# Performance work log

Hardware: AMD Instinct MI355X
Metric: run time of the kernel (lower is better)

Reference implementation:

```python
import jax, jax.numpy as jnp
import numpy as np

N_V, N_H, T, B = 1024, 512, 128, 256


def setup_inputs() -> dict:
    key = jax.random.key(0)
    k = jax.random.split(key, 3)
    v_data = (jax.random.uniform(k[0], (N_V, T, B)) < 0.5).astype(jnp.float32)  # binary visibles
    W = 0.01 * jax.random.normal(k[1], (N_H, N_V), jnp.float32)
    U = 0.01 * jax.random.normal(k[2], (N_H, N_H), jnp.float32)
    b_h = jnp.zeros((N_H,), jnp.float32)
    b_init = jnp.zeros((N_H,), jnp.float32)
    b_v = jnp.zeros((N_V,), jnp.float32)
    return {"v_data": v_data, "W": W, "U": U, "b_h": b_h, "b_init": b_init,
            "b_v": b_v, "CDk": 2}


def _sample_r_over_time(v, W, U, b_h, b_init):
    # v: (V,T,B) -> r: (H,T,B). Sequential mean-field recurrence over T
    # (RTRBM._sample_r_given_v_over_time: t=0 uses b_init and U=0, t>0 uses U,b_h).
    Wv = jnp.einsum('hv,vtb->thb', W, v)  # (T,H,B)
    r0 = jax.nn.sigmoid(Wv[0] + b_init[:, None])

    def step(r_lag, wv_t):
        r_t = jax.nn.sigmoid(wv_t + U @ r_lag + b_h[:, None])
        return r_t, r_t

    _, rs = jax.lax.scan(step, r0, Wv[1:])
    r = jnp.concatenate([r0[None], rs], axis=0)  # (T,H,B)
    return jnp.transpose(r, (1, 0, 2))  # (H,T,B)


def _parallel_r(v, r_lagged, W, U, b_h, b_init):
    # RTRBM._parallel_sample_r_h_given_v probabilities; v:(V,T,B), r_lagged:(H,T,B)
    r0 = jax.nn.sigmoid(jnp.einsum('hv,vb->hb', W, v[:, 0]) + b_init[:, None])
    rr = jax.nn.sigmoid(jnp.einsum('hv,vtb->htb', W, v[:, 1:])
                        + jnp.einsum('hr,rtb->htb', U, r_lagged[:, :-1])
                        + b_h[:, None, None])
    return jnp.concatenate([r0[:, None], rr], axis=1)  # (H,T,B)


def reference(v_data, W, U, b_h, b_init, b_v, CDk):
    key = jax.random.key(42)
    r_data = _sample_r_over_time(v_data, W, U, b_h, b_init)
    key, sk = jax.random.split(key)
    h_model = jax.random.bernoulli(sk, _parallel_r(v_data, r_data, W, U, b_h, b_init)).astype(v_data.dtype)
    for _ in range(CDk - 1):  # CD-k Gibbs chain (CDk is a concrete Python int)
        key, k1, k2 = jax.random.split(key, 3)
        v_prob = jax.nn.sigmoid(jnp.einsum('hv,htb->vtb', W, h_model) + b_v[:, None, None])
        v_model = jax.random.bernoulli(k1, v_prob).astype(v_data.dtype)
        h_model = jax.random.bernoulli(k2, _parallel_r(v_model, r_data, W, U, b_h, b_init)).astype(v_data.dtype)
    key, kf = jax.random.split(key)
    v_model = jax.random.bernoulli(
        kf, jax.nn.sigmoid(jnp.einsum('hv,htb->vtb', W, h_model) + b_v[:, None, None])
    ).astype(v_data.dtype)
    return (v_model, r_data)
```

## Files before the change

### kernel.cpp

```cpp
#include <hip/hip_runtime.h>
#include <hip/hip_bf16.h>
#include <stdint.h>

typedef unsigned long long u64;
typedef uint32_t u32;
typedef __attribute__((ext_vector_type(8))) short bf16x8;
typedef __attribute__((ext_vector_type(4))) float f32x4;

#define NV 1024
#define NH 512
#define TT 128
#define BB 256
#define TBsz (TT*BB)
#define HTBsz (NH*TBsz)
#define VTBsz (NV*TBsz)
#define NWV (NV/64)
#define NWH (NH/64)
#define QCAP 1048576u
#define DELTA 5e-4

__host__ __device__ inline void tf2x32(uint32_t k0, uint32_t k1,
                                       uint32_t x0, uint32_t x1,
                                       uint32_t& o0, uint32_t& o1) {
  const uint32_t ks2 = k0 ^ k1 ^ 0x1BD11BDAu;
#define ROTL(x,d) (((x)<<(d))|((x)>>(32-(d))))
#define RND(r) { x0 += x1; x1 = ROTL(x1,r); x1 ^= x0; }
  x0 += k0;  x1 += k1;
  RND(13) RND(15) RND(26) RND(6)
  x0 += k1;  x1 += ks2 + 1u;
  RND(17) RND(29) RND(16) RND(24)
  x0 += ks2; x1 += k0 + 2u;
  RND(13) RND(15) RND(26) RND(6)
  x0 += k0;  x1 += k1 + 3u;
  RND(17) RND(29) RND(16) RND(24)
  x0 += k1;  x1 += ks2 + 4u;
  RND(13) RND(15) RND(26) RND(6)
  x0 += ks2; x1 += k0 + 5u;
  o0 = x0; o1 = x1;
#undef RND
#undef ROTL
}

__device__ inline double tf_uniform64(uint32_t k0, uint32_t k1, uint32_t i) {
  uint32_t o0, o1;
  tf2x32(k0, k1, 0u, i, o0, o1);
  uint32_t bits = o0 ^ o1;
  uint32_t fb = (bits >> 9) | 0x3f800000u;
  float f = __uint_as_float(fb) - 1.0f;
  return (double)f;
}

__device__ inline double sigmoid64(double x) { return 1.0 / (1.0 + exp(-x)); }

__device__ inline void bfsplit(float w, ushort& b1o, ushort& b2o) {
  __hip_bfloat16 b1 = __float2bfloat16(w);
  float r = w - __bfloat162float(b1);
  __hip_bfloat16 b2 = __float2bfloat16(r);
  b1o = *reinterpret_cast<ushort*>(&b1);
  b2o = *reinterpret_cast<ushort*>(&b2);
}

__global__ __launch_bounds__(256) void kprepWall(const float* __restrict__ W,
                                                 double* __restrict__ W64,
                                                 ushort* __restrict__ A1,
                                                 ushort* __restrict__ A2,
                                                 ushort* __restrict__ AW1,
                                                 ushort* __restrict__ AW2) {
  int idx = blockIdx.x * 256 + threadIdx.x;
  W64[idx] = (double)W[idx];
  {
    int i    = idx & 7;
    int lane = (idx >> 3) & 63;
    int ks   = (idx >> 9) & 15;
    int vt   = idx >> 13;
    int h = ks*32 + ((lane >> 4) << 3) + i;
    int v = vt*16 + (lane & 15);
    bfsplit(W[(size_t)h*NV + v], A1[idx], A2[idx]);
  }
  {
    int i    = idx & 7;
    int lane = (idx >> 3) & 63;
    int kt   = (idx >> 9) & 31;
    int ht   = idx >> 14;
    int h = ht*16 + (lane & 15);
    int v = kt*32 + ((lane >> 4) << 3) + i;
    bfsplit(W[(size_t)h*NV + v], AW1[idx], AW2[idx]);
  }
}

__global__ __launch_bounds__(256) void kprepUall(const float* __restrict__ U,
                                                 double* __restrict__ U64,
                                                 float4* __restrict__ UB,
                                                 ushort* __restrict__ AU1,
                                                 ushort* __restrict__ AU2) {
  int idx = blockIdx.x * 256 + threadIdx.x;
  U64[idx] = (double)U[idx];
  {
    int i    = idx & 7;
    int lane = (idx >> 3) & 63;
    int kt   = (idx >> 9) & 15;
    int ht   = idx >> 13;
    int h = ht*16 + (lane & 15);
    int r = kt*32 + ((lane >> 4) << 3) + i;
    bfsplit(U[(size_t)h*NH + r], AU1[idx], AU2[idx]);
  }
  if (idx < NH*NH/4) {
    int r4 = idx / NH;
    int h  = idx % NH;
    const float* __restrict__ p = U + (size_t)h*NH + r4*4;
    UB[idx] = make_float4(p[0], p[1], p[2], p[3]);
  }
}

__global__ __launch_bounds__(256) void kpack_f32(const float* __restrict__ in,
                                                 u64* __restrict__ out) {
  int tb = blockIdx.x * 256 + threadIdx.x;
  for (int w = 0; w < NWV; ++w) {
    u64 m = 0;
    #pragma unroll 8
    for (int j = 0; j < 64; ++j)
      m |= (u64)(in[(size_t)(w*64 + j)*TBsz + tb] != 0.0f ? 1 : 0) << j;
    out[(size_t)tb*NWV + w] = m;
  }
}

__global__ __launch_bounds__(256) void kWv(const u64* __restrict__ vb,
                                           const double* __restrict__ W64,
                                           double* __restrict__ WvT) {
  const int HM = 8;
  int t  = blockIdx.x / (NH/HM);
  int h0 = (blockIdx.x % (NH/HM)) * HM;
  int tb = t*BB + threadIdx.x;
  u64 m[NWV];
  #pragma unroll
  for (int w = 0; w < NWV; ++w) m[w] = vb[(size_t)tb*NWV + w];
  double acc[HM];
  #pragma unroll
  for (int i = 0; i < HM; ++i) acc[i] = 0.0;
  const double2* __restrict__ W2 = (const double2*)W64;
  for (int w = 0; w < NWV; ++w) {
    u64 mw = m[w];
    #pragma unroll 8
    for (int j2 = 0; j2 < 32; ++j2) {
      double bd0 = (double)((unsigned)((mw >> (2*j2+0)) & 1ull));
      double bd1 = (double)((unsigned)((mw >> (2*j2+1)) & 1ull));
      int vi = w*32 + j2;
      #pragma unroll
      for (int i = 0; i < HM; ++i) {
        double2 wv = W2[(size_t)(h0+i)*(NV/2) + vi];
        acc[i] = fma(bd0, wv.x, acc[i]);
        acc[i] = fma(bd1, wv.y, acc[i]);
      }
    }
  }
  #pragma unroll
  for (int i = 0; i < HM; ++i)
    WvT[(size_t)tb*NH + h0 + i] = acc[i];
}

__global__ __launch_bounds__(512) void krecur(const double* __restrict__ WvT,
                                              const float4* __restrict__ UB,
                                              const float* __restrict__ bh,
                                              const float* __restrict__ binit,
                                              double* __restrict__ rT) {
  __shared__ double rA[2][NH];
  const int b = blockIdx.x;
  const int h = threadIdx.x;
  const double bhd = (double)bh[h];
  double p = sigmoid64(WvT[(size_t)b*NH + h] + (double)binit[h]);
  rA[0][h] = p;
  rT[(size_t)b*NH + h] = p;
  __syncthreads();
  int cur = 0;
  for (int t = 1; t < TT; ++t) {
    double acc = WvT[((size_t)t*BB + b)*NH + h];
    double a0=0, a1=0, a2=0, a3=0;
    const double2* __restrict__ xl = (const double2*)rA[cur];
    const double2* __restrict__ xg =
        (const double2*)(rT + ((size_t)(t-1)*BB + b)*NH);
    #pragma unroll 4
    for (int r = 0; r < 256; r += 4) {
      float4 u4 = UB[(size_t)(r >> 2)*NH + h];
      double2 q01 = xl[(r>>1)+0];
      double2 q23 = xl[(r>>1)+1];
      a0 = fma((double)u4.x, q01.x, a0);
      a1 = fma((double)u4.y, q01.y, a1);
      a2 = fma((double)u4.z, q23.x, a2);
      a3 = fma((double)u4.w, q23.y, a3);
    }
    #pragma unroll 4
    for (int r = 256; r < 512; r += 4) {
      float4 u4 = UB[(size_t)(r >> 2)*NH + h];
      double2 q01 = xg[(r>>1)+0];
      double2 q23 = xg[(r>>1)+1];
      a0 = fma((double)u4.x, q01.x, a0);
      a1 = fma((double)u4.y, q01.y, a1);
      a2 = fma((double)u4.z, q23.x, a2);
      a3 = fma((double)u4.w, q23.y, a3);
    }
    p = sigmoid64((acc + ((a0+a1)+(a2+a3))) + bhd);
    rA[cur ^ 1][h] = p;
    rT[((size_t)t*BB + b)*NH + h] = p;
    __syncthreads();
    cur ^= 1;
  }
}

__global__ __launch_bounds__(256) void ktrans_s(const double* __restrict__ rT,
                                                float* __restrict__ out_r,
                                                uint8_t* __restrict__ hbytes,
                                                u32 k0, u32 k1) {
  __shared__ double lds[32][33];
  int t  = blockIdx.x;
  int h0 = blockIdx.y * 32;
  int b0 = blockIdx.z * 32;
  int tx = threadIdx.x & 31;
  int ty = threadIdx.x >> 5;
  #pragma unroll
  for (int i = 0; i < 4; ++i) {
    int row = ty*4 + i;
    lds[row][tx] = rT[((size_t)t*BB + b0 + row)*NH + h0 + tx];
  }
  __syncthreads();
  #pragma unroll
  for (int i = 0; i < 4; ++i) {
    int row = ty*4 + i;
    out_r[(size_t)(h0+row)*TBsz + (size_t)t*BB + b0 + tx] = (float)lds[tx][row];
  }
  if (threadIdx.x < 128) {
    int tbr = threadIdx.x >> 2;
    int bix = threadIdx.x & 3;
    int tb  = t*BB + b0 + tbr;
    unsigned byte = 0;
    #pragma unroll
    for (int j = 0; j < 8; ++j) {
      int hrel = bix*8 + j;
      double p = lds[tbr][hrel];
      double u = tf_uniform64(k0, k1, (u32)((h0 + hrel)*TBsz + tb));
      byte |= (u < p) ? (1u << j) : 0u;
    }
    hbytes[(size_t)tb*(NH/8) + (h0 >> 3) + bix] = (uint8_t)byte;
  }
}

__global__ __launch_bounds__(256) void kvisM(
    const ushort* __restrict__ A1, const ushort* __restrict__ A2,
    const float* __restrict__ bv, const u64* __restrict__ hbits,
    u64* __restrict__ vbits, float* __restrict__ vf,
    u32* __restrict__ queue, u32* __restrict__ cnt, u32 k0, u32 k1) {
  __shared__ ushort Blds[64*512];
  int nblk = blockIdx.x & 511;
  int vblk = blockIdx.x >> 9;
  int tb0 = nblk * 64, v0 = vblk * 64;
  int tid = threadIdx.x;
  {
    int c = tid >> 2, seg = tid & 3;
    const u64* hp = hbits + (size_t)(tb0 + c)*NWH + seg*2;
    #pragma unroll
    for (int half = 0; half < 2; ++half) {
      u64 mm = hp[half];
      int kbase = seg*128 + half*64;
      #pragma unroll
      for (int j2 = 0; j2 < 32; ++j2) {
        int k = kbase + 2*j2;
        u32 val = (u32)((mm >> (2*j2)) & 1ull) * 0x3F80u
                | (u32)((mm >> (2*j2+1)) & 1ull) * 0x3F800000u;
        int blk = (k >> 3) ^ (c & 7);
        *(u32*)&Blds[c*512 + (blk << 3) + (k & 7)] = val;
      }
    }
  }
  __syncthreads();
  int wv = tid >> 6, l = tid & 63;
  int wr = wv >> 1, wc = wv & 1;
  f32x4 acc[2][2];
  #pragma unroll
  for (int m = 0; m < 2; ++m)
    #pragma unroll
    for (int n = 0; n < 2; ++n) acc[m][n] = (f32x4){0.f,0.f,0.f,0.f};
  for (int ks = 0; ks < 16; ++ks) {
    bf16x8 bf[2];
    #pragma unroll
    for (int n = 0; n < 2; ++n) {
      int col = wc*32 + n*16 + (l & 15);
      int k = ks*32 + ((l >> 4) << 3);
      int blk = (k >> 3) ^ (col & 7);
      bf[n] = *(const bf16x8*)&Blds[col*512 + (blk << 3)];
    }
    #pragma unroll
    for (int m = 0; m < 2; ++m) {
      int vt = vblk*4 + wr*2 + m;
      size_t abase = (((size_t)vt*16 + ks)*64 + l)*8;
      bf16x8 a1 = *(const bf16x8*)&A1[abase];
      bf16x8 a2 = *(const bf16x8*)&A2[abase];
      #pragma unroll
      for (int n = 0; n < 2; ++n) {
        acc[m][n] = __builtin_amdgcn_mfma_f32_16x16x32_bf16(a1, bf[n], acc[m][n], 0,0,0);
        acc[m][n] = __builtin_amdgcn_mfma_f32_16x16x32_bf16(a2, bf[n], acc[m][n], 0,0,0);
      }
    }
  }
  u64 mask[2] = {0, 0};
  int coln[2];
  #pragma unroll
  for (int n = 0; n < 2; ++n) {
    int col = wc*32 + n*16 + (l & 15);
    coln[n] = col;
    int tb = tb0 + col;
    #pragma unroll
    for (int m = 0; m < 2; ++m) {
      #pragma unroll
      for (int r = 0; r < 4; ++r) {
        int vrel = wr*32 + m*16 + ((l >> 4) << 2) + r;
        int v = v0 + vrel;
        float p = 1.f / (1.f + __expf(-(acc[m][n][r] + bv[v])));
        size_t o = (size_t)v*TBsz + tb;
        double u = tf_uniform64(k0, k1, (u32)o);
        double diff = (double)p - u;
        unsigned smp = diff > 0.0 ? 1u : 0u;
        if (fabs(diff) < DELTA) {
          u32 s = atomicAdd(cnt, 1u);
          if (s < QCAP) queue[s] = (u32)o;
        }
        if (smp) mask[n] |= 1ull << vrel;
        if (vf) vf[o] = (float)smp;
      }
    }
  }
  if (vbits) {
    __syncthreads();
    u64* sbits = (u64*)Blds;
    if (tid < 64) sbits[tid] = 0;
    __syncthreads();
    atomicOr(&sbits[coln[0]], mask[0]);
    atomicOr(&sbits[coln[1]], mask[1]);
    __syncthreads();
    if (tid < 64)
      vbits[(size_t)(tb0 + tid)*NWV + (v0 >> 6)] = sbits[tid];
  }
}

__global__ __launch_bounds__(256) void khidM(
    const ushort* __restrict__ AW1, const ushort* __restrict__ AW2,
    const ushort* __restrict__ AU1, const ushort* __restrict__ AU2,
    const float* __restrict__ bh, const float* __restrict__ binit,
    const u64* __restrict__ vbits, const float* __restrict__ r32,
    u64* __restrict__ h2bits, u32* __restrict__ queue,
    u32* __restrict__ cnt, u32 k0, u32 k1) {
  __shared__ ushort Blds[64*512];
  int nblk = blockIdx.x & 511;
  int hblk = blockIdx.x >> 9;
  int tb0 = nblk * 64, h0 = hblk * 64;
  int t = tb0 >> 8;
  int tid = threadIdx.x;
  int wv = tid >> 6, l = tid & 63;
  int wr = wv >> 1, wc = wv & 1;
  f32x4 acc[2][2];
  #pragma unroll
  for (int m = 0; m < 2; ++m)
    #pragma unroll
    for (int n = 0; n < 2; ++n) acc[m][n] = (f32x4){0.f,0.f,0.f,0.f};

  for (int q = 0; q < 2; ++q) {
    {
      int c = tid >> 2, seg = tid & 3;
      const u64* vp = vbits + (size_t)(tb0 + c)*NWV + q*8 + seg*2;
      #pragma unroll
      for (int half = 0; half < 2; ++half) {
        u64 mm = vp[half];
        int kbase = seg*128 + half*64;
        #pragma unroll
        for (int j2 = 0; j2 < 32; ++j2) {
          int k = kbase + 2*j2;
          u32 val = (u32)((mm >> (2*j2)) & 1ull) * 0x3F80u
                  | (u32)((mm >> (2*j2+1)) & 1ull) * 0x3F800000u;
          int blk = (k >> 3) ^ (c & 7);
          *(u32*)&Blds[c*512 + (blk << 3) + (k & 7)] = val;
        }
      }
    }
    __syncthreads();
    for (int ks = 0; ks < 16; ++ks) {
      int kt = q*16 + ks;
      bf16x8 bf[2];
      #pragma unroll
      for (int n = 0; n < 2; ++n) {
        int col = wc*32 + n*16 + (l & 15);
        int k = ks*32 + ((l >> 4) << 3);
        int blk = (k >> 3) ^ (col & 7);
        bf[n] = *(const bf16x8*)&Blds[col*512 + (blk << 3)];
      }
      #pragma unroll
      for (int m = 0; m < 2; ++m) {
        int ht = hblk*4 + wr*2 + m;
        size_t abase = (((size_t)ht*32 + kt)*64 + l)*8;
        bf16x8 a1 = *(const bf16x8*)&AW1[abase];
        bf16x8 a2 = *(const bf16x8*)&AW2[abase];
        #pragma unroll
        for (int n = 0; n < 2; ++n) {
          acc[m][n] = __builtin_amdgcn_mfma_f32_16x16x32_bf16(a1, bf[n], acc[m][n], 0,0,0);
          acc[m][n] = __builtin_amdgcn_mfma_f32_16x16x32_bf16(a2, bf[n], acc[m][n], 0,0,0);
        }
      }
    }
    __syncthreads();
  }

  if (t > 0) {
    int tbl0 = tb0 - 256;
    for (int pl = 0; pl < 2; ++pl) {
      {
        int c  = tid & 63;
        int q4 = tid >> 6;
        const float* __restrict__ rp = r32 + tbl0 + c;
        for (int rr = 0; rr < 128; ++rr) {
          int r = q4*128 + rr;
          float x = rp[(size_t)r*TBsz];
          __hip_bfloat16 b1 = __float2bfloat16(x);
          ushort ub;
          if (pl == 0) {
            ub = *reinterpret_cast<ushort*>(&b1);
          } else {
            float res = x - __bfloat162float(b1);
            __hip_bfloat16 b2 = __float2bfloat16(res);
            ub = *reinterpret_cast<ushort*>(&b2);
          }
          int blk = (r >> 3) ^ (c & 7);
          Blds[c*512 + (blk << 3) + (r & 7)] = ub;
        }
      }
      __syncthreads();
      for (int ks = 0; ks < 16; ++ks) {
        bf16x8 bf[2];
        #pragma unroll
        for (int n = 0; n < 2; ++n) {
          int col = wc*32 + n*16 + (l & 15);
          int k = ks*32 + ((l >> 4) << 3);
          int blk = (k >> 3) ^ (col & 7);
          bf[n] = *(const bf16x8*)&Blds[col*512 + (blk << 3)];
        }
        #pragma unroll
        for (int m = 0; m < 2; ++m) {
          int ht = hblk*4 + wr*2 + m;
          size_t abase = (((size_t)ht*16 + ks)*64 + l)*8;
          bf16x8 a1 = *(const bf16x8*)&AU1[abase];
          bf16x8 a2 = *(const bf16x8*)&AU2[abase];
          #pragma unroll
          for (int n = 0; n < 2; ++n) {
            acc[m][n] = __builtin_amdgcn_mfma_f32_16x16x32_bf16(a1, bf[n], acc[m][n], 0,0,0);
            acc[m][n] = __builtin_amdgcn_mfma_f32_16x16x32_bf16(a2, bf[n], acc[m][n], 0,0,0);
          }
        }
      }
      __syncthreads();
    }
  }

  const float* __restrict__ bias = (t > 0) ? bh : binit;
  u64 mask[2] = {0, 0};
  int coln[2];
  #pragma unroll
  for (int n = 0; n < 2; ++n) {
    int col = wc*32 + n*16 + (l & 15);
    coln[n] = col;
    int tb = tb0 + col;
    #pragma unroll
    for (int m = 0; m < 2; ++m) {
      #pragma unroll
      for (int r = 0; r < 4; ++r) {
        int hrel = wr*32 + m*16 + ((l >> 4) << 2) + r;
        int h = h0 + hrel;
        float p = 1.f / (1.f + __expf(-(acc[m][n][r] + bias[h])));
        size_t o = (size_t)h*TBsz + tb;
        double u = tf_uniform64(k0, k1, (u32)o);
        double diff = (double)p - u;
        unsigned smp = diff > 0.0 ? 1u : 0u;
        if (fabs(diff) < DELTA) {
          u32 s = atomicAdd(cnt, 1u);
          if (s < QCAP) queue[s] = (u32)o;
        }
        if (smp) mask[n] |= 1ull << hrel;
      }
    }
  }
  __syncthreads();
  u64* sbits = (u64*)Blds;
  if (tid < 64) sbits[tid] = 0;
  __syncthreads();
  atomicOr(&sbits[coln[0]], mask[0]);
  atomicOr(&sbits[coln[1]], mask[1]);
  __syncthreads();
  if (tid < 64)
    h2bits[(size_t)(tb0 + tid)*NWH + hblk] = sbits[tid];
}

__global__ __launch_bounds__(256) void kvis_fix(
    const float* __restrict__ W, const float* __restrict__ bv,
    const u64* __restrict__ hbits, u64* __restrict__ fixbits,
    float* __restrict__ vf, const u32* __restrict__ queue,
    const u32* __restrict__ cnt, u32 k0, u32 k1) {
  u32 n = *cnt; if (n > QCAP) n = QCAP;
  for (u32 q = blockIdx.x*256 + threadIdx.x; q < n; q += gridDim.x*256) {
    u32 o = queue[q];
    u32 v = o / TBsz, tb = o % TBsz;
    double a0=0, a1=0, a2=0, a3=0;
    for (int w = 0; w < NWH; ++w) {
      u64 mw = hbits[(size_t)tb*NWH + w];
      for (int j = 0; j < 64; j += 4) {
        if ((mw >> (j+0)) & 1ull) a0 += (double)W[(size_t)(w*64+j+0)*NV + v];
        if ((mw >> (j+1)) & 1ull) a1 += (double)W[(size_t)(w*64+j+1)*NV + v];
        if ((mw >> (j+2)) & 1ull) a2 += (double)W[(size_t)(w*64+j+2)*NV + v];
        if ((mw >> (j+3)) & 1ull) a3 += (double)W[(size_t)(w*64+j+3)*NV + v];
      }
    }
    double p = sigmoid64(((a0+a1)+(a2+a3)) + (double)bv[v]);
    double u = tf_uniform64(k0, k1, o);
    unsigned smp = (u < p) ? 1u : 0u;
    if (vf) vf[o] = (float)smp;
    if (fixbits) {
      size_t wi = (size_t)tb*NWV + (v >> 6);
      unsigned bit = v & 63u;
      unsigned cur = (unsigned)((fixbits[wi] >> bit) & 1ull);
      if (cur != smp) atomicXor(&fixbits[wi], 1ull << bit);
    }
  }
}

__global__ __launch_bounds__(256) void khid_fix(
    const u64* __restrict__ vbits, const float* __restrict__ W,
    const double* __restrict__ U64, const float* __restrict__ bh,
    const float* __restrict__ binit, const double* __restrict__ rT,
    u64* __restrict__ fixbits, const u32* __restrict__ queue,
    const u32* __restrict__ cnt, u32 k0, u32 k1) {
  u32 n = *cnt; if (n > QCAP) n = QCAP;
  for (u32 q = blockIdx.x*256 + threadIdx.x; q < n; q += gridDim.x*256) {
    u32 o = queue[q];
    u32 h = o / TBsz, tb = o % TBsz;
    u32 t = tb / BB, b = tb % BB;
    double a0=0, a1=0, a2=0, a3=0;
    for (int w = 0; w < NWV; ++w) {
      u64 mw = vbits[(size_t)tb*NWV + w];
      for (int j = 0; j < 64; j += 4) {
        if ((mw >> (j+0)) & 1ull) a0 += (double)W[(size_t)h*NV + w*64+j+0];
        if ((mw >> (j+1)) & 1ull) a1 += (double)W[(size_t)h*NV + w*64+j+1];
        if ((mw >> (j+2)) & 1ull) a2 += (double)W[(size_t)h*NV + w*64+j+2];
        if ((mw >> (j+3)) & 1ull) a3 += (double)W[(size_t)h*NV + w*64+j+3];
      }
    }
    double logit = (a0+a1) + (a2+a3);
    if (t > 0) {
      const double* __restrict__ rp = rT + ((size_t)(t-1)*BB + b)*NH;
      const double* __restrict__ Ur = U64 + (size_t)h*NH;
      double u0=0, u1=0, u2=0, u3=0;
      for (int r = 0; r < NH; r += 4) {
        u0 = fma(Ur[r+0], rp[r+0], u0);
        u1 = fma(Ur[r+1], rp[r+1], u1);
        u2 = fma(Ur[r+2], rp[r+2], u2);
        u3 = fma(Ur[r+3], rp[r+3], u3);
      }
      logit = (logit + ((u0+u1)+(u2+u3))) + (double)bh[h];
    } else {
      logit += (double)binit[h];
    }
    double p = sigmoid64(logit);
    double u = tf_uniform64(k0, k1, o);
    unsigned smp = (u < p) ? 1u : 0u;
    size_t wi = (size_t)tb*NWH + (h >> 6);
    unsigned bit = h & 63u;
    unsigned cur = (unsigned)((fixbits[wi] >> bit) & 1ull);
    if (cur != smp) atomicXor(&fixbits[wi], 1ull << bit);
  }
}

extern "C" void kernel_launch(void* const* d_in, const int* in_sizes, int n_in,
                              void* d_out, int out_size, void* d_ws, size_t ws_size,
                              hipStream_t stream) {
  const float* vd    = (const float*)d_in[0];
  const float* W     = (const float*)d_in[1];
  const float* U     = (const float*)d_in[2];
  const float* bh    = (const float*)d_in[3];
  const float* binit = (const float*)d_in[4];
  const float* bv    = (const float*)d_in[5];

  float* out_v = (float*)d_out;
  float* out_r = (float*)d_out + VTBsz;
  double* WvT = (double*)d_out;

  char* w = (char*)d_ws;
  double* rT    = (double*)w;  w += (size_t)HTBsz*8;
  u64* vdbits   = (u64*)w;     w += (size_t)TBsz*NWV*8;
  u64* v1bits   = (u64*)w;     w += (size_t)TBsz*NWV*8;
  u64* h1bits   = (u64*)w;     w += (size_t)TBsz*NWH*8;
  u64* h2bits   = (u64*)w;     w += (size_t)TBsz*NWH*8;
  double* W64   = (double*)w;  w += (size_t)NH*NV*8;
  double* U64   = (double*)w;  w += (size_t)NH*NH*8;
  float4* UB    = (float4*)w;  w += (size_t)NH*NH*4;
  ushort* A1    = (ushort*)w;  w += (size_t)NH*NV*2;
  ushort* A2    = (ushort*)w;  w += (size_t)NH*NV*2;
  ushort* AW1   = (ushort*)w;  w += (size_t)NH*NV*2;
  ushort* AW2   = (ushort*)w;  w += (size_t)NH*NV*2;
  ushort* AU1   = (ushort*)w;  w += (size_t)NH*NH*2;
  ushort* AU2   = (ushort*)w;  w += (size_t)NH*NH*2;
  u32* q0       = (u32*)w;     w += (size_t)QCAP*4;
  u32* q1       = (u32*)w;     w += (size_t)QCAP*4;
  u32* q2       = (u32*)w;     w += (size_t)QCAP*4;
  u32* cnt      = (u32*)w;     w += 256;
  (void)ws_size; (void)in_sizes; (void)n_in; (void)out_size;

  uint32_t ka0,ka1, sk0,sk1;
  tf2x32(0u,42u, 0u,0u, ka0,ka1);
  tf2x32(0u,42u, 0u,1u, sk0,sk1);
  uint32_t kb0,kb1, k10,k11, k20,k21;
  tf2x32(ka0,ka1, 0u,0u, kb0,kb1);
  tf2x32(ka0,ka1, 0u,1u, k10,k11);
  tf2x32(ka0,ka1, 0u,2u, k20,k21);
  uint32_t kc0,kc1, kf0,kf1;
  tf2x32(kb0,kb1, 0u,0u, kc0,kc1);
  tf2x32(kb0,kb1, 0u,1u, kf0,kf1);

  hipMemsetAsync(cnt, 0, 3*sizeof(u32), stream);

  kprepWall<<<(NH*NV)/256, 256, 0, stream>>>(W, W64, A1, A2, AW1, AW2);
  kprepUall<<<(NH*NH)/256, 256, 0, stream>>>(U, U64, UB, AU1, AU2);
  kpack_f32<<<TBsz/256, 256, 0, stream>>>(vd, vdbits);

  kWv<<<TT*(NH/8), 256, 0, stream>>>(vdbits, W64, WvT);

  krecur<<<BB, NH, 0, stream>>>(WvT, UB, bh, binit, rT);

  ktrans_s<<<dim3(TT, NH/32, BB/32), 256, 0, stream>>>(rT, out_r,
                                                       (uint8_t*)h1bits, sk0, sk1);

  kvisM<<<16*512, 256, 0, stream>>>(A1, A2, bv, h1bits, v1bits, nullptr,
                                    q0, cnt+0, k10, k11);
  kvis_fix<<<128, 256, 0, stream>>>(W, bv, h1bits, v1bits, nullptr,
                                    q0, cnt+0, k10, k11);

  khidM<<<8*512, 256, 0, stream>>>(AW1, AW2, AU1, AU2, bh, binit,
                                   v1bits, out_r, h2bits, q1, cnt+1, k20, k21);
  khid_fix<<<128, 256, 0, stream>>>(v1bits, W, U64, bh, binit, rT,
                                    h2bits, q1, cnt+1, k20, k21);

  kvisM<<<16*512, 256, 0, stream>>>(A1, A2, bv, h2bits, nullptr, out_v,
                                    q2, cnt+2, kf0, kf1);
  kvis_fix<<<128, 256, 0, stream>>>(W, bv, h2bits, nullptr, out_v,
                                    q2, cnt+2, kf0, kf1);
}
```

Measured before the change: 5.745 ms.

## Make kvisM loop over all visible blocks per column tile and use LDS in recurrence

kvisM now gives each block 128 tb columns and loops over all 16 visible blocks, so the unpacked hidden-bit tile in LDS is built once and reused across the whole visible dimension. The old version rebuilt a 64-column tile for every (v-block, column-block) pair. The launch shrinks to 256 blocks, each holding about 128KB of LDS, so each CU likely runs a single block of 4 waves with little latency hiding. Separately, the recurrence kernel now reads the whole previous r vector from LDS instead of taking half of it from global memory.

```diff
diff --git a/kernel.cpp b/kernel.cpp
--- a/kernel.cpp
+++ b/kernel.cpp
@@ -175,24 +175,12 @@
   for (int t = 1; t < TT; ++t) {
     double acc = WvT[((size_t)t*BB + b)*NH + h];
     double a0=0, a1=0, a2=0, a3=0;
-    const double2* __restrict__ xl = (const double2*)rA[cur];
-    const double2* __restrict__ xg =
-        (const double2*)(rT + ((size_t)(t-1)*BB + b)*NH);
+    const double2* __restrict__ rA2 = (const double2*)rA[cur];
     #pragma unroll 4
-    for (int r = 0; r < 256; r += 4) {
+    for (int r = 0; r < NH; r += 4) {
       float4 u4 = UB[(size_t)(r >> 2)*NH + h];
-      double2 q01 = xl[(r>>1)+0];
-      double2 q23 = xl[(r>>1)+1];
-      a0 = fma((double)u4.x, q01.x, a0);
-      a1 = fma((double)u4.y, q01.y, a1);
-      a2 = fma((double)u4.z, q23.x, a2);
-      a3 = fma((double)u4.w, q23.y, a3);
-    }
-    #pragma unroll 4
-    for (int r = 256; r < 512; r += 4) {
-      float4 u4 = UB[(size_t)(r >> 2)*NH + h];
-      double2 q01 = xg[(r>>1)+0];
-      double2 q23 = xg[(r>>1)+1];
+      double2 q01 = rA2[(r>>1)+0];
+      double2 q23 = rA2[(r>>1)+1];
       a0 = fma((double)u4.x, q01.x, a0);
       a1 = fma((double)u4.y, q01.y, a1);
       a2 = fma((double)u4.z, q23.x, a2);
@@ -248,18 +236,18 @@
     const float* __restrict__ bv, const u64* __restrict__ hbits,
     u64* __restrict__ vbits, float* __restrict__ vf,
     u32* __restrict__ queue, u32* __restrict__ cnt, u32 k0, u32 k1) {
-  __shared__ ushort Blds[64*512];
-  int nblk = blockIdx.x & 511;
-  int vblk = blockIdx.x >> 9;
-  int tb0 = nblk * 64, v0 = vblk * 64;
+  __shared__ ushort Blds[128*512];
+  __shared__ u64 sbits[128];
+  int tb0 = blockIdx.x * 128;
   int tid = threadIdx.x;
   {
-    int c = tid >> 2, seg = tid & 3;
-    const u64* hp = hbits + (size_t)(tb0 + c)*NWH + seg*2;
+    int c  = tid & 127;
+    int hs = tid >> 7;
+    const u64* hp = hbits + (size_t)(tb0 + c)*NWH + hs*4;
     #pragma unroll
-    for (int half = 0; half < 2; ++half) {
-      u64 mm = hp[half];
-      int kbase = seg*128 + half*64;
+    for (int w = 0; w < 4; ++w) {
+      u64 mm = hp[w];
+      int kbase = hs*256 + w*64;
       #pragma unroll
       for (int j2 = 0; j2 < 32; ++j2) {
         int k = kbase + 2*j2;
@@ -273,70 +261,73 @@
   __syncthreads();
   int wv = tid >> 6, l = tid & 63;
   int wr = wv >> 1, wc = wv & 1;
-  f32x4 acc[2][2];
-  #pragma unroll
-  for (int m = 0; m < 2; ++m)
+  for (int vblk = 0; vblk < 16; ++vblk) {
+    f32x4 acc[2][4];
     #pragma unroll
-    for (int n = 0; n < 2; ++n) acc[m][n] = (f32x4){0.f,0.f,0.f,0.f};
-  for (int ks = 0; ks < 16; ++ks) {
-    bf16x8 bf[2];
+    for (int m = 0; m < 2; ++m)
+      #pragma unroll
+      for (int n = 0; n < 4; ++n) acc[m][n] = (f32x4){0.f,0.f,0.f,0.f};
+    for (int ks = 0; ks < 16; ++ks) {
+      bf16x8 bf[4];
+      #pragma unroll
+      for (int n = 0; n < 4; ++n) {
+        int col = wc*64 + n*16 + (l & 15);
+        int k = ks*32 + ((l >> 4) << 3);
+        int blk = (k >> 3) ^ (col & 7);
+        bf[n] = *(const bf16x8*)&Blds[col*512 + (blk << 3)];
+      }
+      #pragma unroll
+      for (int m = 0; m < 2; ++m) {
+        int vt = vblk*4 + wr*2 + m;
+        size_t abase = (((size_t)vt*16 + ks)*64 + l)*8;
+        bf16x8 a1 = *(const bf16x8*)&A1[abase];
+        bf16x8 a2 = *(const bf16x8*)&A2[abase];
+        #pragma unroll
+        for (int n = 0; n < 4; ++n) {
+          acc[m][n] = __builtin_amdgcn_mfma_f32_16x16x32_bf16(a1, bf[n], acc[m][n], 0,0,0);
+          acc[m][n] = __builtin_amdgcn_mfma_f32_16x16x32_bf16(a2, bf[n], acc[m][n], 0,0,0);
+        }
+      }
+    }
+    int v0 = vblk * 64;
+    u64 mask[4] = {0,0,0,0};
     #pragma unroll
-    for (int n = 0; n < 2; ++n) {
-      int col = wc*32 + n*16 + (l & 15);
-      int k = ks*32 + ((l >> 4) << 3);
-      int blk = (k >> 3) ^ (col & 7);
-      bf[n] = *(const bf16x8*)&Blds[col*512 + (blk << 3)];
-    }
-    #pragma unroll
-    for (int m = 0; m < 2; ++m) {
-      int vt = vblk*4 + wr*2 + m;
-      size_t abase = (((size_t)vt*16 + ks)*64 + l)*8;
-      bf16x8 a1 = *(const bf16x8*)&A1[abase];
-      bf16x8 a2 = *(const bf16x8*)&A2[abase];
-      #pragma unroll
-      for (int n = 0; n < 2; ++n) {
-        acc[m][n] = __builtin_amdgcn_mfma_f32_16x16x32_bf16(a1, bf[n], acc[m][n], 0,0,0);
-        acc[m][n] = __builtin_amdgcn_mfma_f32_16x16x32_bf16(a2, bf[n], acc[m][n], 0,0,0);
-      }
-    }
-  }
-  u64 mask[2] = {0, 0};
-  int coln[2];
-  #pragma unroll
-  for (int n = 0; n < 2; ++n) {
-    int col = wc*32 + n*16 + (l & 15);
-    coln[n] = col;
-    int tb = tb0 + col;
-    #pragma unroll
-    for (int m = 0; m < 2; ++m) {
-      #pragma unroll
-      for (int r = 0; r < 4; ++r) {
-        int vrel = wr*32 + m*16 + ((l >> 4) << 2) + r;
-        int v = v0 + vrel;
-        float p = 1.f / (1.f + __expf(-(acc[m][n][r] + bv[v])));
-        size_t o = (size_t)v*TBsz + tb;
-        double u = tf_uniform64(k0, k1, (u32)o);
-        double diff = (double)p - u;
-        unsigned smp = diff > 0.0 ? 1u : 0u;
-        if (fabs(diff) < DELTA) {
-          u32 s = atomicAdd(cnt, 1u);
-          if (s < QCAP) queue[s] = (u32)o;
-        }
-        if (smp) mask[n] |= 1ull << vrel;
-        if (vf) vf[o] = (float)smp;
-      }
-    }
-  }
-  if (vbits) {
-    __syncthreads();
-    u64* sbits = (u64*)Blds;
-    if (tid < 64) sbits[tid] = 0;
-    __syncthreads();
-    atomicOr(&sbits[coln[0]], mask[0]);
-    atomicOr(&sbits[coln[1]], mask[1]);
-    __syncthreads();
-    if (tid < 64)
-      vbits[(size_t)(tb0 + tid)*NWV + (v0 >> 6)] = sbits[tid];
+    for (int n = 0; n < 4; ++n) {
+      int col = wc*64 + n*16 + (l & 15);
+      int tb = tb0 + col;
+      #pragma unroll
+      for (int m = 0; m < 2; ++m) {
+        #pragma unroll
+        for (int r = 0; r < 4; ++r) {
+          int vrel = wr*32 + m*16 + ((l >> 4) << 2) + r;
+          int v = v0 + vrel;
+          float p = 1.f / (1.f + __expf(-(acc[m][n][r] + bv[v])));
+          size_t o = (size_t)v*TBsz + tb;
+          double u = tf_uniform64(k0, k1, (u32)o);
+          double diff = (double)p - u;
+          unsigned smp = diff > 0.0 ? 1u : 0u;
+          if (fabs(diff) < DELTA) {
+            u32 s = atomicAdd(cnt, 1u);
+            if (s < QCAP) queue[s] = (u32)o;
+          }
+          if (smp) mask[n] |= 1ull << vrel;
+          if (vf) vf[o] = (float)smp;
+        }
+      }
+    }
+    if (vbits) {
+      __syncthreads();
+      if (tid < 128) sbits[tid] = 0;
+      __syncthreads();
+      #pragma unroll
+      for (int n = 0; n < 4; ++n) {
+        int col = wc*64 + n*16 + (l & 15);
+        atomicOr(&sbits[col], mask[n]);
+      }
+      __syncthreads();
+      if (tid < 128)
+        vbits[(size_t)(tb0 + tid)*NWV + vblk] = sbits[tid];
+    }
   }
 }
 
@@ -631,8 +622,8 @@
   ktrans_s<<<dim3(TT, NH/32, BB/32), 256, 0, stream>>>(rT, out_r,
                                                        (uint8_t*)h1bits, sk0, sk1);
 
-  kvisM<<<16*512, 256, 0, stream>>>(A1, A2, bv, h1bits, v1bits, nullptr,
-                                    q0, cnt+0, k10, k11);
+  kvisM<<<TBsz/128, 256, 0, stream>>>(A1, A2, bv, h1bits, v1bits, nullptr,
+                                      q0, cnt+0, k10, k11);
   kvis_fix<<<128, 256, 0, stream>>>(W, bv, h1bits, v1bits, nullptr,
                                     q0, cnt+0, k10, k11);
 
@@ -641,8 +632,8 @@
   khid_fix<<<128, 256, 0, stream>>>(v1bits, W, U64, bh, binit, rT,
                                     h2bits, q1, cnt+1, k20, k21);
 
-  kvisM<<<16*512, 256, 0, stream>>>(A1, A2, bv, h2bits, nullptr, out_v,
-                                    q2, cnt+2, kf0, kf1);
+  kvisM<<<TBsz/128, 256, 0, stream>>>(A1, A2, bv, h2bits, nullptr, out_v,
+                                      q2, cnt+2, kf0, kf1);
   kvis_fix<<<128, 256, 0, stream>>>(W, bv, h2bits, nullptr, out_v,
                                     q2, cnt+2, kf0, kf1);
 }
```

Result: faster. 5.144 ms (-10.5%).
